# Kernel tuning notes

Hardware: AMD Instinct MI355X
Metric: run time of the kernel (lower is better)

Reference implementation:

```python
import jax, jax.numpy as jnp
import numpy as np

B, D = 8, 128
CH = [1, 2, 4, 8, 16, 32, 64]
STRIDES = [1, 2, 2, 2, 2, 2]
EPS = 1e-5


def setup_inputs() -> dict:
    key = jax.random.key(0)
    ks = jax.random.split(key, 8)
    inp = {
        'x_feats': jax.random.normal(ks[0], (B, D, D, D, 1), jnp.float32),
        'x_mask': jax.random.randint(ks[1], (B, D, D, D, 1), 0, 2).astype(jnp.int32),
    }
    for i in range(6):
        cin, cout = CH[i], CH[i + 1]
        inp[f'w{i}'] = jax.random.normal(ks[2 + i], (3, 3, 3, cin, cout), jnp.float32) * (1.0 / np.sqrt(27.0 * cin))
        inp[f'g{i}'] = jnp.ones((cout,), jnp.float32)
        inp[f'b{i}'] = jnp.zeros((cout,), jnp.float32)
    return inp


def _conv(x, w, stride):
    # x: [B,D,D,D,Cin], w: [3,3,3,Cin,Cout]; SAME-style pad=1 so output index p gathers stride*p + {-1,0,1}
    return jax.lax.conv_general_dilated(
        x, w, (stride,) * 3, [(1, 1)] * 3,
        dimension_numbers=('NDHWC', 'DHWIO', 'NDHWC'))


def _down_mask(m):
    # ME strided coord map: out coord p active iff any input coord c with floor(c/2)==p is active
    return jax.lax.reduce_window(m, 0.0, jax.lax.max,
                                 (1, 2, 2, 2, 1), (1, 2, 2, 2, 1), 'VALID')


def _bn_relu(x, m, g, b):
    # batch-norm over ACTIVE voxels only (x is already zero at inactive sites)
    cnt = jnp.maximum(jnp.sum(m), 1.0)
    mean = jnp.sum(x, axis=(0, 1, 2, 3)) / cnt            # [C]
    var = jnp.sum(x * x, axis=(0, 1, 2, 3)) / cnt - mean * mean
    y = (x - mean) * (g * jax.lax.rsqrt(var + EPS)) + b
    return jnp.maximum(y, 0.0) * m


def _forward(x_feats, x_mask, ws, gs, bs):
    m = x_mask.astype(x_feats.dtype)
    x = x_feats * m
    for i in range(6):
        x = _conv(x, ws[i], STRIDES[i])
        if STRIDES[i] == 2:
            m = _down_mask(m)
        x = x * m  # zero values at inactive output coords (sparse tensor semantics)
        x = _bn_relu(x, m, gs[i], bs[i])
    # sparse max pooling k=3 s=2: max over active inputs in footprint 2p+{-1,0,1}
    neg = jnp.asarray(-jnp.inf, x.dtype)
    filled = jnp.where(m > 0, x, neg)
    pooled = jax.lax.reduce_window(filled, neg, jax.lax.max,
                                   (1, 3, 3, 3, 1), (1, 2, 2, 2, 1),
                                   [(0, 0), (1, 1), (1, 1), (1, 1), (0, 0)])
    mo = _down_mask(m)
    return jnp.where(mo > 0, pooled, 0.0)  # [B, 2, 2, 2, 64]


def reference(x_feats, x_mask, w0, w1, w2, w3, w4, w5,
              g0, g1, g2, g3, g4, g5, b0, b1, b2, b3, b4, b5):
    ws = [w0, w1, w2, w3, w4, w5]
    gs = [g0, g1, g2, g3, g4, g5]
    bs = [b0, b1, b2, b3, b4, b5]
    return _forward(x_feats, x_mask, ws, gs, bs)
```

## Files before the change

### kernel.cpp

```cpp
#include <hip/hip_runtime.h>
#include <hip/hip_bf16.h>
#include <stdint.h>

#define DEV __device__ __forceinline__

constexpr int BATCH = 8;

constexpr int il2(int n) { return (n <= 1) ? 0 : 1 + il2(n / 2); }

DEV float ldy(const float* p, int i) { return p[i]; }
DEV float ldy(const __hip_bfloat16* p, int i) { return __bfloat162float(p[i]); }
DEV void sty(float* p, size_t i, float v) { p[i] = v; }
DEV void sty(__hip_bfloat16* p, size_t i, float v) { p[i] = __float2bfloat16(v); }

DEV uint32_t f2bf(float v) {
  __hip_bfloat16 h = __float2bfloat16(v);
  return (uint32_t)*reinterpret_cast<uint16_t*>(&h);
}
DEV float bflo(uint32_t u) {
  uint32_t t = u << 16;
  float f;
  __builtin_memcpy(&f, &t, 4);
  return f;
}
DEV float bfhi(uint32_t u) {
  uint32_t t = u & 0xffff0000u;
  float f;
  __builtin_memcpy(&f, &t, 4);
  return f;
}
constexpr uint32_t NEGINF_BF = 0xFF80u;
DEV int xswz(int o, int nwg) { return (o & 7) * (nwg >> 3) + (o >> 3); }

__global__ __launch_bounds__(256) void maskA_k(const int* __restrict__ msk,
                                               uint8_t* __restrict__ m0,
                                               uint8_t* __restrict__ m1,
                                               uint8_t* __restrict__ m2) {
  __shared__ uint8_t t0[32768];
  __shared__ uint8_t t1[4096];
  int blk = blockIdx.x;
  int bx = (blk & 3) * 32, by = ((blk >> 2) & 3) * 32, bz = ((blk >> 4) & 3) * 32, b = blk >> 6;
  int tid = threadIdx.x;
  for (int g = tid; g < 8192; g += 256) {
    int gx4 = (g & 7) * 4, gy = (g >> 3) & 31, gz = g >> 8;
    int gidx = ((b * 128 + bz + gz) * 128 + by + gy) * 128 + bx + gx4;
    int4 v = *(const int4*)(msk + gidx);
    uint32_t o = (v.x ? 1u : 0u) | (v.y ? 256u : 0u) | (v.z ? 65536u : 0u) | (v.w ? 16777216u : 0u);
    ((uint32_t*)t0)[g] = o;
    ((uint32_t*)m0)[gidx >> 2] = o;
  }
  __syncthreads();
  for (int j = tid; j < 4096; j += 256) {
    int ox = j & 15, oy = (j >> 4) & 15, oz = j >> 8;
    uint32_t act = 0;
#pragma unroll
    for (int dz = 0; dz < 2; dz++)
#pragma unroll
      for (int dy = 0; dy < 2; dy++)
        act |= *(const uint16_t*)&t0[(2 * oz + dz) * 1024 + (2 * oy + dy) * 32 + 2 * ox];
    uint8_t vv = act ? 1 : 0;
    t1[j] = vv;
    m1[((b * 64 + bz / 2 + oz) * 64 + by / 2 + oy) * 64 + bx / 2 + ox] = vv;
  }
  __syncthreads();
  for (int j = tid; j < 512; j += 256) {
    int ox = j & 7, oy = (j >> 3) & 7, oz = j >> 6;
    uint32_t act = 0;
#pragma unroll
    for (int dz = 0; dz < 2; dz++)
#pragma unroll
      for (int dy = 0; dy < 2; dy++)
        act |= *(const uint16_t*)&t1[(2 * oz + dz) * 256 + (2 * oy + dy) * 16 + 2 * ox];
    m2[((b * 32 + bz / 4 + oz) * 32 + by / 4 + oy) * 32 + bx / 4 + ox] = act ? 1 : 0;
  }
}

__global__ __launch_bounds__(1024) void maskB_k(const uint8_t* __restrict__ m2,
                                                uint8_t* __restrict__ m3,
                                                uint8_t* __restrict__ m4,
                                                uint8_t* __restrict__ m5,
                                                uint8_t* __restrict__ m6) {
  __shared__ uint8_t t3[32768];
  __shared__ uint8_t t4[4096];
  __shared__ uint8_t t5[512];
  int tid = threadIdx.x;
  for (int j = tid; j < 32768; j += 1024) {
    int ox = j & 15, oy = (j >> 4) & 15, oz = (j >> 8) & 15, b = j >> 12;
    uint32_t act = 0;
#pragma unroll
    for (int dz = 0; dz < 2; dz++)
#pragma unroll
      for (int dy = 0; dy < 2; dy++)
        act |= *(const uint16_t*)&m2[((b * 32 + 2 * oz + dz) * 32 + 2 * oy + dy) * 32 + 2 * ox];
    uint8_t v = act ? 1 : 0;
    t3[j] = v;
    m3[j] = v;
  }
  __syncthreads();
  for (int j = tid; j < 4096; j += 1024) {
    int ox = j & 7, oy = (j >> 3) & 7, oz = (j >> 6) & 7, b = j >> 9;
    uint32_t act = 0;
#pragma unroll
    for (int dz = 0; dz < 2; dz++)
#pragma unroll
      for (int dy = 0; dy < 2; dy++)
        act |= *(const uint16_t*)&t3[((b * 16 + 2 * oz + dz) * 16 + 2 * oy + dy) * 16 + 2 * ox];
    uint8_t v = act ? 1 : 0;
    t4[j] = v;
    m4[j] = v;
  }
  __syncthreads();
  if (tid < 512) {
    int j = tid;
    int ox = j & 3, oy = (j >> 2) & 3, oz = (j >> 4) & 3, b = j >> 6;
    uint32_t act = 0;
#pragma unroll
    for (int dz = 0; dz < 2; dz++)
#pragma unroll
      for (int dy = 0; dy < 2; dy++)
        act |= *(const uint16_t*)&t4[((b * 8 + 2 * oz + dz) * 8 + 2 * oy + dy) * 8 + 2 * ox];
    uint8_t v = act ? 1 : 0;
    t5[j] = v;
    m5[j] = v;
  }
  __syncthreads();
  if (tid < 64) {
    int j = tid;
    int ox = j & 1, oy = (j >> 1) & 1, oz = (j >> 2) & 1, b = j >> 3;
    uint32_t act = 0;
#pragma unroll
    for (int dz = 0; dz < 2; dz++)
#pragma unroll
      for (int dy = 0; dy < 2; dy++)
        act |= *(const uint16_t*)&t5[((b * 4 + 2 * oz + dz) * 4 + 2 * oy + dy) * 4 + 2 * ox];
    m6[j] = act ? 1 : 0;
  }
}

__global__ __launch_bounds__(256, 4) void conv0_k(const float* __restrict__ x,
                                                  const uint8_t* __restrict__ m0,
                                                  const float* __restrict__ w,
                                                  __hip_bfloat16* __restrict__ y0,
                                                  float* __restrict__ partials) {
  constexpr int NROW = 180;
  constexpr int ROUNDS = 6;
  __shared__ float sx[3240];
  __shared__ float sm[4][5];
  int blk = xswz(blockIdx.x, 8192);
  int tx0 = (blk & 7) * 16, ty0 = ((blk >> 3) & 7) * 16, tz0 = ((blk >> 6) & 15) * 8,
      b = blk >> 10;
  int tid = threadIdx.x;
  int q = tid & 7, rowb = tid >> 3;

  float4 xq[ROUNDS];
  uint32_t mq[ROUNDS];
#pragma unroll
  for (int r = 0; r < ROUNDS; r++) {
    int row = rowb + 32 * r;
    int sz = row / 18;
    int sy = row - sz * 18;
    int gz = tz0 + sz - 1, gy = ty0 + sy - 1;
    int gx4 = tx0 - 4 + 4 * q;
    bool in = (row < NROW) & ((unsigned)gz < 128u) & ((unsigned)gy < 128u) &
              ((unsigned)gx4 < 128u);
    int gi = in ? ((b * 128 + gz) * 128 + gy) * 128 + gx4 : 0;
    xq[r] = *(const float4*)(x + gi);
    uint32_t mr = *(const uint32_t*)(m0 + gi);
    mq[r] = in ? mr : 0u;
  }
#pragma unroll
  for (int r = 0; r < ROUNDS; r++) {
    int row = rowb + 32 * r;
    if (row >= NROW) continue;
    float vals[4] = {xq[r].x, xq[r].y, xq[r].z, xq[r].w};
    uint32_t mw = mq[r];
#pragma unroll
    for (int e = 0; e < 4; e++) {
      int col = 4 * q - 3 + e;
      if ((unsigned)col < 18u)
        sx[row * 18 + col] = ((mw >> (8 * e)) & 0xffu) ? vals[e] : 0.f;
    }
  }
  __syncthreads();

  int tc = tid & 7, tb = (tid >> 3) & 7, ta = tid >> 6;
  int lx = tc * 2, ly = tb * 2, lz = ta * 2;

  uint32_t mm[2][2];
#pragma unroll
  for (int oz = 0; oz < 2; oz++)
#pragma unroll
    for (int oy = 0; oy < 2; oy++) {
      int z = tz0 + lz + oz, y = ty0 + ly + oy, xx = tx0 + lx;
      mm[oz][oy] = *(const uint16_t*)(m0 + ((b * 128 + z) * 128 + y) * 128 + xx);
    }

  float acc[2][2][2][2];
#pragma unroll
  for (int oz = 0; oz < 2; oz++)
#pragma unroll
    for (int oy = 0; oy < 2; oy++)
#pragma unroll
      for (int ox = 0; ox < 2; ox++)
        acc[oz][oy][ox][0] = acc[oz][oy][ox][1] = 0.f;

#pragma unroll
  for (int p = 0; p < 4; p++) {
    float pl[4][4];
#pragma unroll
    for (int yy = 0; yy < 4; yy++)
#pragma unroll
      for (int xx2 = 0; xx2 < 4; xx2 += 2) {
        float2 v = *(const float2*)&sx[(lz + p) * 324 + (ly + yy) * 18 + lx + xx2];
        pl[yy][xx2] = v.x;
        pl[yy][xx2 + 1] = v.y;
      }
#pragma unroll
    for (int oz = 0; oz < 2; oz++) {
      int dz = p - oz;
      if (dz < 0 || dz > 2) continue;
#pragma unroll
      for (int dy = 0; dy < 3; dy++)
#pragma unroll
        for (int dx = 0; dx < 3; dx++) {
          float w0 = w[((dz * 3 + dy) * 3 + dx) * 2];
          float w1 = w[((dz * 3 + dy) * 3 + dx) * 2 + 1];
#pragma unroll
          for (int oy = 0; oy < 2; oy++)
#pragma unroll
            for (int ox = 0; ox < 2; ox++) {
              float s = pl[oy + dy][ox + dx];
              acc[oz][oy][ox][0] = fmaf(s, w0, acc[oz][oy][ox][0]);
              acc[oz][oy][ox][1] = fmaf(s, w1, acc[oz][oy][ox][1]);
            }
        }
    }
  }

  float s0 = 0.f, q0 = 0.f, s1 = 0.f, q1 = 0.f;
  int cnt = 0;
#pragma unroll
  for (int oz = 0; oz < 2; oz++)
#pragma unroll
    for (int oy = 0; oy < 2; oy++) {
      int z = tz0 + lz + oz, y = ty0 + ly + oy, xx = tx0 + lx;
      int vo = ((b * 128 + z) * 128 + y) * 128 + xx;
      uint32_t m2b = mm[oz][oy];
      uint2 st;
      if (m2b & 0xff) {
        st.x = f2bf(acc[oz][oy][0][0]) | (f2bf(acc[oz][oy][0][1]) << 16);
        s0 += acc[oz][oy][0][0];
        q0 += acc[oz][oy][0][0] * acc[oz][oy][0][0];
        s1 += acc[oz][oy][0][1];
        q1 += acc[oz][oy][0][1] * acc[oz][oy][0][1];
        cnt++;
      } else {
        st.x = NEGINF_BF | (NEGINF_BF << 16);
      }
      if (m2b >> 8) {
        st.y = f2bf(acc[oz][oy][1][0]) | (f2bf(acc[oz][oy][1][1]) << 16);
        s0 += acc[oz][oy][1][0];
        q0 += acc[oz][oy][1][0] * acc[oz][oy][1][0];
        s1 += acc[oz][oy][1][1];
        q1 += acc[oz][oy][1][1] * acc[oz][oy][1][1];
        cnt++;
      } else {
        st.y = NEGINF_BF | (NEGINF_BF << 16);
      }
      ((uint2*)y0)[vo >> 1] = st;
    }
  float cf = (float)cnt;
#pragma unroll
  for (int off = 32; off >= 1; off >>= 1) {
    s0 += __shfl_xor(s0, off);
    q0 += __shfl_xor(q0, off);
    s1 += __shfl_xor(s1, off);
    q1 += __shfl_xor(q1, off);
    cf += __shfl_xor(cf, off);
  }
  int wave = tid >> 6;
  if ((tid & 63) == 0) {
    sm[wave][0] = s0;
    sm[wave][1] = q0;
    sm[wave][2] = s1;
    sm[wave][3] = q1;
    sm[wave][4] = cf;
  }
  __syncthreads();
  if (tid < 5) {
    float t = 0.f;
#pragma unroll
    for (int wv = 0; wv < 4; wv++) t += sm[wv][tid];
    partials[blk * 5 + tid] = t;
  }
}

template <int Din, int Cin, int Cout, int TZ, typename Tin, typename Tout>
__global__ __launch_bounds__(64 * TZ, 4) void conv_tile_k(const Tin* __restrict__ yin,
                                                          const uint8_t* __restrict__ mo,
                                                          const float* __restrict__ ssin,
                                                          const float* __restrict__ w,
                                                          Tout* __restrict__ yout,
                                                          float* __restrict__ partials) {
  static_assert(sizeof(Tin) == 2 && (Cin == 2 || Cin == 4), "bf16 input only");
  constexpr int Dout = Din / 2;
  constexpr int NT = 64 * TZ;
  constexpr int IZ = 2 * TZ + 1;
  constexpr int NROW = 17 * IZ;
  constexpr int NPAIR = NROW * 9;
  constexpr int PR = (NPAIR + NT - 1) / NT;
  constexpr int TXN = Dout / 8;
  constexpr int TZN = Dout / TZ;
  constexpr int LTX = il2(TXN);
  constexpr int LTZ = il2(TZN);
  constexpr int NWG = TXN * TXN * TZN * BATCH;
  constexpr int REC = 2 * Cout + 1;
  __shared__ float sx[289 * IZ * Cin];
  __shared__ float sm[TZ][REC];

  int tid = threadIdx.x;
  int blk = xswz(blockIdx.x, NWG);
  int tx0 = (blk & (TXN - 1)) * 8;
  int ty0 = ((blk >> LTX) & (TXN - 1)) * 8;
  int tz0 = ((blk >> (2 * LTX)) & (TZN - 1)) * TZ;
  int b = blk >> (2 * LTX + LTZ);

  float sc[Cin], sh[Cin];
#pragma unroll
  for (int ci = 0; ci < Cin; ci++) {
    sc[ci] = ssin[2 * ci];
    sh[ci] = ssin[2 * ci + 1];
  }

  int oy0 = 2 * ty0 - 1, oz0 = 2 * tz0 - 1;
  uint2 pv2[PR];
  uint4 pv4[PR];
  uint32_t okb = 0;
#pragma unroll
  for (int r = 0; r < PR; r++) {
    int i = tid + r * NT;
    int row = i / 9, qq = i - 9 * row;
    int sz = row / 17, sy = row - 17 * sz;
    int gz = oz0 + sz, gy = oy0 + sy;
    int px = 2 * tx0 - 2 + 2 * qq;
    bool ok = (i < NPAIR) & ((unsigned)gz < (unsigned)Din) & ((unsigned)gy < (unsigned)Din) &
              (px >= 0);
    int gi = ok ? ((b * Din + gz) * Din + gy) * Din + px : 0;
    if (ok) okb |= (1u << r);
    if constexpr (Cin == 2)
      pv2[r] = *(const uint2*)((const uint16_t*)yin + (size_t)gi * 2);
    else
      pv4[r] = *(const uint4*)((const uint16_t*)yin + (size_t)gi * 4);
  }
#pragma unroll
  for (int r = 0; r < PR; r++) {
    int i = tid + r * NT;
    if (i >= NPAIR) continue;
    int row = i / 9, qq = i - 9 * row;
    bool ok = (okb >> r) & 1u;
#pragma unroll
    for (int e = 0; e < 2; e++) {
      int u = 2 * qq - 1 + e;
      if ((unsigned)u >= 17u) continue;
      int site = row * 17 + u;
      if constexpr (Cin == 2) {
        uint32_t vv = e ? pv2[r].y : pv2[r].x;
        float f0 = ok ? fmaxf(fmaf(bflo(vv), sc[0], sh[0]), 0.f) : 0.f;
        float f1 = ok ? fmaxf(fmaf(bfhi(vv), sc[1], sh[1]), 0.f) : 0.f;
        *(float2*)&sx[site * 2] = make_float2(f0, f1);
      } else {
        uint32_t va = e ? pv4[r].z : pv4[r].x;
        uint32_t vb = e ? pv4[r].w : pv4[r].y;
        float f0 = ok ? fmaxf(fmaf(bflo(va), sc[0], sh[0]), 0.f) : 0.f;
        float f1 = ok ? fmaxf(fmaf(bfhi(va), sc[1], sh[1]), 0.f) : 0.f;
        float f2 = ok ? fmaxf(fmaf(bflo(vb), sc[2], sh[2]), 0.f) : 0.f;
        float f3 = ok ? fmaxf(fmaf(bfhi(vb), sc[3], sh[3]), 0.f) : 0.f;
        *(float4*)&sx[site * 4] = make_float4(f0, f1, f2, f3);
      }
    }
  }
  __syncthreads();

  int tc = tid & 7, tb = (tid >> 3) & 7, ta = tid >> 6;
  int lx = tc, ly = tb, lz = ta;
  int vo = ((b * Dout + tz0 + lz) * Dout + ty0 + ly) * Dout + tx0 + lx;
  bool act = mo[vo] != 0;
  float acc[Cout];
#pragma unroll
  for (int co = 0; co < Cout; co++) acc[co] = 0.f;
  if (act) {
    int base = ((2 * lz) * 289 + (2 * ly) * 17 + (2 * lx)) * Cin;
#pragma unroll
    for (int dz = 0; dz < 3; dz++)
#pragma unroll
      for (int dy = 0; dy < 3; dy++)
#pragma unroll
        for (int dx = 0; dx < 3; dx++) {
          int off = base + (dz * 289 + dy * 17 + dx) * Cin;
          const float* wp = w + ((dz * 3 + dy) * 3 + dx) * Cin * Cout;
#pragma unroll
          for (int ci = 0; ci < Cin; ci++) {
            float s = sx[off + ci];
#pragma unroll
            for (int co = 0; co < Cout; co++)
              acc[co] = fmaf(s, wp[ci * Cout + co], acc[co]);
          }
        }
  }
  {
    uint32_t pk[Cout / 2];
    if (act) {
#pragma unroll
      for (int k = 0; k < Cout / 2; k++) pk[k] = f2bf(acc[2 * k]) | (f2bf(acc[2 * k + 1]) << 16);
    } else {
#pragma unroll
      for (int k = 0; k < Cout / 2; k++) pk[k] = NEGINF_BF | (NEGINF_BF << 16);
    }
    if constexpr (Cout == 4)
      *(uint2*)((uint16_t*)yout + (size_t)vo * 4) = *(uint2*)pk;
    else if constexpr (Cout == 8)
      *(uint4*)((uint16_t*)yout + (size_t)vo * 8) = *(uint4*)pk;
    else {
#pragma unroll
      for (int k = 0; k < Cout / 2; k++)
        *((uint32_t*)yout + (size_t)vo * (Cout / 2) + k) = pk[k];
    }
  }
  unsigned long long bal = __ballot(act);
  int wave = tid >> 6, lane = tid & 63;
#pragma unroll
  for (int co = 0; co < Cout; co++) {
    float s = acc[co], q = acc[co] * acc[co];
#pragma unroll
    for (int off = 32; off >= 1; off >>= 1) {
      s += __shfl_xor(s, off);
      q += __shfl_xor(q, off);
    }
    if (lane == 0) {
      sm[wave][2 * co] = s;
      sm[wave][2 * co + 1] = q;
    }
  }
  if (lane == 0) sm[wave][2 * Cout] = (float)__popcll(bal);
  __syncthreads();
  if (tid < REC) {
    float t = 0.f;
#pragma unroll
    for (int wv = 0; wv < TZ; wv++) t += sm[wv][tid];
    partials[(size_t)blk * REC + tid] = t;
  }
}

template <int Din, int Cin, int Cout, typename Tin, typename Tout>
__global__ __launch_bounds__(256) void conv_s2_k(const Tin* __restrict__ yin,
                                                 const uint8_t* __restrict__ mo,
                                                 const float* __restrict__ ssin,
                                                 const float* __restrict__ w,
                                                 Tout* __restrict__ yout,
                                                 float* __restrict__ partials) {
  constexpr int Dout = Din / 2;
  constexpr int LD = il2(Dout);
  constexpr int LC = il2(Cout);
  constexpr int REC = 2 * Cout + 1;
  int tid = threadIdx.x;
  int lin = blockIdx.x * 256 + tid;
  int co = lin & (Cout - 1);
  int v = lin >> LC;
  int x = v & (Dout - 1);
  int y = (v >> LD) & (Dout - 1);
  int z = (v >> (2 * LD)) & (Dout - 1);
  int b = v >> (3 * LD);
  bool act = mo[v] != 0;
  float acc = 0.f;
  if (act) {
    for (int dz = 0; dz < 3; dz++) {
      int iz = 2 * z + dz - 1;
      if ((unsigned)iz >= (unsigned)Din) continue;
      for (int dy = 0; dy < 3; dy++) {
        int iy = 2 * y + dy - 1;
        if ((unsigned)iy >= (unsigned)Din) continue;
        for (int dx = 0; dx < 3; dx++) {
          int ix = 2 * x + dx - 1;
          if ((unsigned)ix >= (unsigned)Din) continue;
          int gi = ((b * Din + iz) * Din + iy) * Din + ix;
          const float* wp = w + ((dz * 3 + dy) * 3 + dx) * Cin * Cout + co;
          float f[Cin];
          if constexpr (sizeof(Tin) == 2 && Cin == 8) {
            uint4 rr = *(const uint4*)((const uint16_t*)yin + (size_t)gi * 8);
            f[0] = bflo(rr.x);
            f[1] = bfhi(rr.x);
            f[2] = bflo(rr.y);
            f[3] = bfhi(rr.y);
            f[4] = bflo(rr.z);
            f[5] = bfhi(rr.z);
            f[6] = bflo(rr.w);
            f[7] = bfhi(rr.w);
          } else if constexpr (sizeof(Tin) == 4 && (Cin % 4) == 0) {
            const float* yp = (const float*)yin + (size_t)gi * Cin;
#pragma unroll
            for (int c4 = 0; c4 < Cin; c4 += 4) {
              float4 vv = *(const float4*)(yp + c4);
              f[c4] = vv.x;
              f[c4 + 1] = vv.y;
              f[c4 + 2] = vv.z;
              f[c4 + 3] = vv.w;
            }
          } else {
            const Tin* yp = yin + (size_t)gi * Cin;
#pragma unroll
            for (int ci = 0; ci < Cin; ci++) f[ci] = ldy(yp, ci);
          }
#pragma unroll
          for (int ci = 0; ci < Cin; ci++) {
            float val = fmaxf(fmaf(f[ci], ssin[2 * ci], ssin[2 * ci + 1]), 0.f);
            acc = fmaf(val, wp[ci * Cout], acc);
          }
        }
      }
    }
  }
  sty(yout, (size_t)lin, act ? acc : -INFINITY);
  float s = acc, q = acc * acc;
#pragma unroll
  for (int off = 32; off >= Cout; off >>= 1) {
    s += __shfl_xor(s, off);
    q += __shfl_xor(q, off);
  }
  unsigned long long bal = __ballot(act && co == 0);
  __shared__ float sm[4][REC];
  int wave = tid >> 6, lane = tid & 63;
  if (lane < Cout) {
    sm[wave][2 * lane] = s;
    sm[wave][2 * lane + 1] = q;
  }
  if (lane == 0) sm[wave][2 * Cout] = (float)__popcll(bal);
  __syncthreads();
  if (tid < REC)
    partials[(size_t)blockIdx.x * REC + tid] = sm[0][tid] + sm[1][tid] + sm[2][tid] + sm[3][tid];
}

template <int Cout>
__global__ __launch_bounds__(256) void stats_k(const float* __restrict__ partials, int nblocks,
                                               const float* __restrict__ g,
                                               const float* __restrict__ bb,
                                               float* __restrict__ ss) {
  constexpr int REC = 2 * Cout + 1;
  int c = blockIdx.x, tid = threadIdx.x;
  float s = 0.f, q = 0.f, n = 0.f;
  for (int i = tid; i < nblocks; i += 256) {
    const float* p = partials + (size_t)i * REC;
    s += p[2 * c];
    q += p[2 * c + 1];
    n += p[2 * Cout];
  }
  __shared__ float S[256], Q[256], N[256];
  S[tid] = s;
  Q[tid] = q;
  N[tid] = n;
  __syncthreads();
  for (int st = 128; st > 0; st >>= 1) {
    if (tid < st) {
      S[tid] += S[tid + st];
      Q[tid] += Q[tid + st];
      N[tid] += N[tid + st];
    }
    __syncthreads();
  }
  if (tid == 0) {
    float cnt = fmaxf(N[0], 1.f);
    float mean = S[0] / cnt;
    float var = Q[0] / cnt - mean * mean;
    float scale = g[c] * rsqrtf(var + 1e-5f);
    ss[2 * c] = scale;
    ss[2 * c + 1] = bb[c] - mean * scale;
  }
}

__global__ __launch_bounds__(512) void pool_stats_k(const float* __restrict__ y5,
                                                    const uint8_t* __restrict__ m6,
                                                    const float* __restrict__ partials,
                                                    const float* __restrict__ g,
                                                    const float* __restrict__ bb,
                                                    float* __restrict__ out) {
  __shared__ float ssc[64], ssh[64];
  int b = blockIdx.x, tid = threadIdx.x;
  if (tid < 64) {
    float s = 0.f, q = 0.f, n = 0.f;
    for (int i = 0; i < 128; i++) {
      const float* p = partials + i * 129;
      s += p[2 * tid];
      q += p[2 * tid + 1];
      n += p[128];
    }
    float cnt = fmaxf(n, 1.f);
    float mean = s / cnt;
    float var = q / cnt - mean * mean;
    float scale = g[tid] * rsqrtf(var + 1e-5f);
    ssc[tid] = scale;
    ssh[tid] = bb[tid] - mean * scale;
  }
  __syncthreads();
  int c = tid & 63, s = tid >> 6;
  int qx = s & 1, qy = (s >> 1) & 1, qz = (s >> 2) & 1;
  int ov = ((b * 2 + qz) * 2 + qy) * 2 + qx;
  float scale = ssc[c], shift = ssh[c];
  float mx = 0.f;
  for (int dz = 0; dz < 3; dz++) {
    int iz = 2 * qz + dz - 1;
    if ((unsigned)iz >= 4u) continue;
    for (int dy = 0; dy < 3; dy++) {
      int iy = 2 * qy + dy - 1;
      if ((unsigned)iy >= 4u) continue;
      for (int dx = 0; dx < 3; dx++) {
        int ix = 2 * qx + dx - 1;
        if ((unsigned)ix >= 4u) continue;
        int gi = ((b * 4 + iz) * 4 + iy) * 4 + ix;
        float val = fmaxf(fmaf(y5[gi * 64 + c], scale, shift), 0.f);
        mx = fmaxf(mx, val);
      }
    }
  }
  out[ov * 64 + c] = m6[ov] ? mx : 0.f;
}

extern "C" void kernel_launch(void* const* d_in, const int* in_sizes, int n_in,
                              void* d_out, int out_size, void* d_ws, size_t ws_size,
                              hipStream_t stream) {
  const float* x = (const float*)d_in[0];
  const int* msk = (const int*)d_in[1];
  const float *w[6], *g[6], *bb[6];
  for (int i = 0; i < 6; i++) {
    w[i] = (const float*)d_in[2 + 3 * i];
    g[i] = (const float*)d_in[3 + 3 * i];
    bb[i] = (const float*)d_in[4 + 3 * i];
  }

  char* ws = (char*)d_ws;
  size_t o = 0;
  auto A = [&](size_t bytes) -> char* {
    char* p = ws + o;
    o = (o + bytes + 255) & ~(size_t)255;
    return p;
  };
  __hip_bfloat16* y0 = (__hip_bfloat16*)A(33554432 * 2);
  __hip_bfloat16* y1 = (__hip_bfloat16*)A(8388608 * 2);
  __hip_bfloat16* y2 = (__hip_bfloat16*)A(2097152 * 2);
  float* y3 = (float*)A(2097152);
  float* y4 = (float*)A(524288);
  float* y5 = (float*)A(131072);
  uint8_t* m0 = (uint8_t*)A(16777216);
  uint8_t* m1 = (uint8_t*)A(2097152);
  uint8_t* m2 = (uint8_t*)A(262144);
  uint8_t* m3 = (uint8_t*)A(32768);
  uint8_t* m4 = (uint8_t*)A(4096);
  uint8_t* m5 = (uint8_t*)A(512);
  uint8_t* m6 = (uint8_t*)A(64);
  float* part = (float*)A(2 << 20);
  float* ss = (float*)A(4096);
  if (o > ws_size) return;

  maskA_k<<<512, 256, 0, stream>>>(msk, m0, m1, m2);
  maskB_k<<<1, 1024, 0, stream>>>(m2, m3, m4, m5, m6);

  conv0_k<<<8192, 256, 0, stream>>>(x, m0, w[0], y0, part);
  stats_k<2><<<2, 256, 0, stream>>>(part, 8192, g[0], bb[0], ss + 0);
  conv_tile_k<128, 2, 4, 4, __hip_bfloat16, __hip_bfloat16>
      <<<8192, 256, 0, stream>>>(y0, m1, ss + 0, w[1], y1, part);
  stats_k<4><<<4, 256, 0, stream>>>(part, 8192, g[1], bb[1], ss + 128);
  conv_tile_k<64, 4, 8, 4, __hip_bfloat16, __hip_bfloat16>
      <<<1024, 256, 0, stream>>>(y1, m2, ss + 128, w[2], y2, part);
  stats_k<8><<<8, 256, 0, stream>>>(part, 1024, g[2], bb[2], ss + 256);
  conv_s2_k<32, 8, 16, __hip_bfloat16, float>
      <<<2048, 256, 0, stream>>>(y2, m3, ss + 256, w[3], y3, part);
  stats_k<16><<<16, 256, 0, stream>>>(part, 2048, g[3], bb[3], ss + 384);
  conv_s2_k<16, 16, 32, float, float>
      <<<512, 256, 0, stream>>>(y3, m4, ss + 384, w[4], y4, part);
  stats_k<32><<<32, 256, 0, stream>>>(part, 512, g[4], bb[4], ss + 512);
  conv_s2_k<8, 32, 64, float, float>
      <<<128, 256, 0, stream>>>(y4, m5, ss + 512, w[5], y5, part);
  pool_stats_k<<<8, 512, 0, stream>>>(y5, m6, part, g[5], bb[5], (float*)d_out);
}
```

Measured before the change: 254.3 us.

## Fuse BN stats and mask downsampling into producer kernels via last-block atomics

Removes the separate maskB and several stats kernels by having the last-finishing block of each producer kernel, found with fenced atomic counters, compute the coarser masks or the BN scale/shift. This cuts kernel launches and the serial gaps between them in a chain of small kernels. It also rewrites conv0's shared-memory staging with a padded row stride and a different thread-to-load mapping. It adds a memset, atomics and a serial tail in one block per kernel.

```diff
diff --git a/kernel.cpp b/kernel.cpp
--- a/kernel.cpp
+++ b/kernel.cpp
@@ -32,12 +32,57 @@
 constexpr uint32_t NEGINF_BF = 0xFF80u;
 DEV int xswz(int o, int nwg) { return (o & 7) * (nwg >> 3) + (o >> 3); }
 
+template <int Cout>
+DEV void fused_stats_body(const float* partials, int nblocks, const float* g,
+                          const float* bb, float* ss, float* red, int tid) {
+  constexpr int LC = il2(Cout);
+  constexpr int REC = 2 * Cout + 1;
+  int c = tid & (Cout - 1);
+  float s = 0.f, q = 0.f, n = 0.f;
+  for (int i = tid >> LC; i < nblocks; i += (256 >> LC)) {
+    const float* p = partials + (size_t)i * REC;
+    s += p[2 * c];
+    q += p[2 * c + 1];
+    n += p[2 * Cout];
+  }
+  float* S = red;
+  float* Q = red + 256;
+  float* N = red + 512;
+  S[tid] = s;
+  Q[tid] = q;
+  N[tid] = n;
+  __syncthreads();
+  for (int st = 128; st >= Cout; st >>= 1) {
+    if (tid < st) {
+      S[tid] += S[tid + st];
+      Q[tid] += Q[tid + st];
+      N[tid] += N[tid + st];
+    }
+    __syncthreads();
+  }
+  if (tid < Cout) {
+    float cnt = fmaxf(N[tid], 1.f);
+    float mean = S[tid] / cnt;
+    float var = Q[tid] / cnt - mean * mean;
+    float scale = g[tid] * rsqrtf(var + 1e-5f);
+    ss[2 * tid] = scale;
+    ss[2 * tid + 1] = bb[tid] - mean * scale;
+  }
+}
+
 __global__ __launch_bounds__(256) void maskA_k(const int* __restrict__ msk,
                                                uint8_t* __restrict__ m0,
                                                uint8_t* __restrict__ m1,
-                                               uint8_t* __restrict__ m2) {
+                                               uint8_t* __restrict__ m2,
+                                               uint8_t* __restrict__ m3,
+                                               uint8_t* __restrict__ m4,
+                                               uint8_t* __restrict__ m5,
+                                               uint8_t* __restrict__ m6,
+                                               int* __restrict__ cnt) {
   __shared__ uint8_t t0[32768];
   __shared__ uint8_t t1[4096];
+  __shared__ uint8_t t5[512];
+  __shared__ int lastf;
   int blk = blockIdx.x;
   int bx = (blk & 3) * 32, by = ((blk >> 2) & 3) * 32, bz = ((blk >> 4) & 3) * 32, b = blk >> 6;
   int tid = threadIdx.x;
@@ -73,67 +118,68 @@
         act |= *(const uint16_t*)&t1[(2 * oz + dz) * 256 + (2 * oy + dy) * 16 + 2 * ox];
     m2[((b * 32 + bz / 4 + oz) * 32 + by / 4 + oy) * 32 + bx / 4 + ox] = act ? 1 : 0;
   }
-}
-
-__global__ __launch_bounds__(1024) void maskB_k(const uint8_t* __restrict__ m2,
-                                                uint8_t* __restrict__ m3,
-                                                uint8_t* __restrict__ m4,
-                                                uint8_t* __restrict__ m5,
-                                                uint8_t* __restrict__ m6) {
-  __shared__ uint8_t t3[32768];
-  __shared__ uint8_t t4[4096];
-  __shared__ uint8_t t5[512];
-  int tid = threadIdx.x;
-  for (int j = tid; j < 32768; j += 1024) {
-    int ox = j & 15, oy = (j >> 4) & 15, oz = (j >> 8) & 15, b = j >> 12;
-    uint32_t act = 0;
-#pragma unroll
-    for (int dz = 0; dz < 2; dz++)
-#pragma unroll
-      for (int dy = 0; dy < 2; dy++)
-        act |= *(const uint16_t*)&m2[((b * 32 + 2 * oz + dz) * 32 + 2 * oy + dy) * 32 + 2 * ox];
-    uint8_t v = act ? 1 : 0;
-    t3[j] = v;
-    m3[j] = v;
-  }
-  __syncthreads();
-  for (int j = tid; j < 4096; j += 1024) {
-    int ox = j & 7, oy = (j >> 3) & 7, oz = (j >> 6) & 7, b = j >> 9;
-    uint32_t act = 0;
-#pragma unroll
-    for (int dz = 0; dz < 2; dz++)
-#pragma unroll
-      for (int dy = 0; dy < 2; dy++)
-        act |= *(const uint16_t*)&t3[((b * 16 + 2 * oz + dz) * 16 + 2 * oy + dy) * 16 + 2 * ox];
-    uint8_t v = act ? 1 : 0;
-    t4[j] = v;
-    m4[j] = v;
-  }
-  __syncthreads();
-  if (tid < 512) {
-    int j = tid;
-    int ox = j & 3, oy = (j >> 2) & 3, oz = (j >> 4) & 3, b = j >> 6;
-    uint32_t act = 0;
-#pragma unroll
-    for (int dz = 0; dz < 2; dz++)
-#pragma unroll
-      for (int dy = 0; dy < 2; dy++)
-        act |= *(const uint16_t*)&t4[((b * 8 + 2 * oz + dz) * 8 + 2 * oy + dy) * 8 + 2 * ox];
-    uint8_t v = act ? 1 : 0;
-    t5[j] = v;
-    m5[j] = v;
-  }
-  __syncthreads();
-  if (tid < 64) {
-    int j = tid;
-    int ox = j & 1, oy = (j >> 1) & 1, oz = (j >> 2) & 1, b = j >> 3;
-    uint32_t act = 0;
-#pragma unroll
-    for (int dz = 0; dz < 2; dz++)
-#pragma unroll
-      for (int dy = 0; dy < 2; dy++)
-        act |= *(const uint16_t*)&t5[((b * 4 + 2 * oz + dz) * 4 + 2 * oy + dy) * 4 + 2 * ox];
-    m6[j] = act ? 1 : 0;
+  __threadfence();
+  __syncthreads();
+  if (tid == 0) {
+    int d = 0;
+    if (atomicAdd(cnt + 32 * (blk & 7), 1) == (512 >> 3) - 1)
+      d = (atomicAdd(cnt + 256, 1) == 7) ? 1 : 0;
+    lastf = d;
+  }
+  __syncthreads();
+  if (lastf) {
+    __threadfence();
+    for (int j = tid; j < 32768; j += 256) {
+      int ox = j & 15, oy = (j >> 4) & 15, oz = (j >> 8) & 15, bb2 = j >> 12;
+      uint32_t act = 0;
+#pragma unroll
+      for (int dz = 0; dz < 2; dz++)
+#pragma unroll
+        for (int dy = 0; dy < 2; dy++)
+          act |= *(const uint16_t*)&m2[((bb2 * 32 + 2 * oz + dz) * 32 + 2 * oy + dy) * 32 + 2 * ox];
+      uint8_t v = act ? 1 : 0;
+      t0[j] = v;
+      m3[j] = v;
+    }
+    __syncthreads();
+    for (int j = tid; j < 4096; j += 256) {
+      int ox = j & 7, oy = (j >> 3) & 7, oz = (j >> 6) & 7, bb2 = j >> 9;
+      uint32_t act = 0;
+#pragma unroll
+      for (int dz = 0; dz < 2; dz++)
+#pragma unroll
+        for (int dy = 0; dy < 2; dy++)
+          act |= *(const uint16_t*)&t0[((bb2 * 16 + 2 * oz + dz) * 16 + 2 * oy + dy) * 16 + 2 * ox];
+      uint8_t v = act ? 1 : 0;
+      t1[j] = v;
+      m4[j] = v;
+    }
+    __syncthreads();
+    for (int j = tid; j < 512; j += 256) {
+      int ox = j & 3, oy = (j >> 2) & 3, oz = (j >> 4) & 3, bb2 = j >> 6;
+      uint32_t act = 0;
+#pragma unroll
+      for (int dz = 0; dz < 2; dz++)
+#pragma unroll
+        for (int dy = 0; dy < 2; dy++)
+          act |= *(const uint16_t*)&t1[((bb2 * 8 + 2 * oz + dz) * 8 + 2 * oy + dy) * 8 + 2 * ox];
+      uint8_t v = act ? 1 : 0;
+      t5[j] = v;
+      m5[j] = v;
+    }
+    __syncthreads();
+    if (tid < 64) {
+      int j = tid;
+      int ox = j & 1, oy = (j >> 1) & 1, oz = (j >> 2) & 1, bb2 = j >> 3;
+      uint32_t act = 0;
+#pragma unroll
+      for (int dz = 0; dz < 2; dz++)
+#pragma unroll
+        for (int dy = 0; dy < 2; dy++)
+          act |= *(const uint16_t*)&t5[((bb2 * 4 + 2 * oz + dz) * 4 + 2 * oy + dy) * 4 + 2 * ox];
+      m6[j] = act ? 1 : 0;
+    }
+    if (tid < 9) cnt[32 * tid] = 0;
   }
 }
 
@@ -142,43 +188,47 @@
                                                   const float* __restrict__ w,
                                                   __hip_bfloat16* __restrict__ y0,
                                                   float* __restrict__ partials) {
+  constexpr int SR = 26;
   constexpr int NROW = 180;
-  constexpr int ROUNDS = 6;
-  __shared__ float sx[3240];
+  constexpr int NTASK = NROW * 6;
+  constexpr int ROUNDS = 5;
+  __shared__ float sx[NROW * SR];
   __shared__ float sm[4][5];
   int blk = xswz(blockIdx.x, 8192);
   int tx0 = (blk & 7) * 16, ty0 = ((blk >> 3) & 7) * 16, tz0 = ((blk >> 6) & 15) * 8,
       b = blk >> 10;
   int tid = threadIdx.x;
-  int q = tid & 7, rowb = tid >> 3;
 
   float4 xq[ROUNDS];
   uint32_t mq[ROUNDS];
 #pragma unroll
   for (int r = 0; r < ROUNDS; r++) {
-    int row = rowb + 32 * r;
-    int sz = row / 18;
-    int sy = row - sz * 18;
-    int gz = tz0 + sz - 1, gy = ty0 + sy - 1;
-    int gx4 = tx0 - 4 + 4 * q;
-    bool in = (row < NROW) & ((unsigned)gz < 128u) & ((unsigned)gy < 128u) &
+    unsigned i = tid + 256u * r;
+    unsigned row = (i * 43691u) >> 18;
+    int k = (int)(i - row * 6u);
+    unsigned sz = (row * 3641u) >> 16;
+    int sy = (int)(row - sz * 18u);
+    int gz = tz0 + (int)sz - 1, gy = ty0 + sy - 1;
+    int gx4 = tx0 - 4 + 4 * k;
+    bool ok = (row < (unsigned)NROW) & ((unsigned)gz < 128u) & ((unsigned)gy < 128u) &
               ((unsigned)gx4 < 128u);
-    int gi = in ? ((b * 128 + gz) * 128 + gy) * 128 + gx4 : 0;
+    int gi = ok ? ((b * 128 + gz) * 128 + gy) * 128 + gx4 : 0;
     xq[r] = *(const float4*)(x + gi);
     uint32_t mr = *(const uint32_t*)(m0 + gi);
-    mq[r] = in ? mr : 0u;
+    mq[r] = ok ? mr : 0u;
   }
 #pragma unroll
   for (int r = 0; r < ROUNDS; r++) {
-    int row = rowb + 32 * r;
-    if (row >= NROW) continue;
-    float vals[4] = {xq[r].x, xq[r].y, xq[r].z, xq[r].w};
-    uint32_t mw = mq[r];
-#pragma unroll
-    for (int e = 0; e < 4; e++) {
-      int col = 4 * q - 3 + e;
-      if ((unsigned)col < 18u)
-        sx[row * 18 + col] = ((mw >> (8 * e)) & 0xffu) ? vals[e] : 0.f;
+    unsigned i = tid + 256u * r;
+    unsigned row = (i * 43691u) >> 18;
+    int k = (int)(i - row * 6u);
+    if (row < (unsigned)NROW) {
+      float vals[4] = {xq[r].x, xq[r].y, xq[r].z, xq[r].w};
+      uint32_t mw = mq[r];
+      int base = (int)row * SR + 4 * k + 1;
+#pragma unroll
+      for (int e = 0; e < 4; e++)
+        sx[base + e] = ((mw >> (8 * e)) & 0xffu) ? vals[e] : 0.f;
     }
   }
   __syncthreads();
@@ -210,10 +260,10 @@
 #pragma unroll
     for (int yy = 0; yy < 4; yy++)
 #pragma unroll
-      for (int xx2 = 0; xx2 < 4; xx2 += 2) {
-        float2 v = *(const float2*)&sx[(lz + p) * 324 + (ly + yy) * 18 + lx + xx2];
-        pl[yy][xx2] = v.x;
-        pl[yy][xx2 + 1] = v.y;
+      for (int j = 0; j < 4; j += 2) {
+        float2 v = *(const float2*)&sx[((lz + p) * 18 + (ly + yy)) * SR + lx + 4 + j];
+        pl[yy][j] = v.x;
+        pl[yy][j + 1] = v.y;
       }
 #pragma unroll
     for (int oz = 0; oz < 2; oz++) {
@@ -238,7 +288,7 @@
   }
 
   float s0 = 0.f, q0 = 0.f, s1 = 0.f, q1 = 0.f;
-  int cnt = 0;
+  int cnt2 = 0;
 #pragma unroll
   for (int oz = 0; oz < 2; oz++)
 #pragma unroll
@@ -253,7 +303,7 @@
         q0 += acc[oz][oy][0][0] * acc[oz][oy][0][0];
         s1 += acc[oz][oy][0][1];
         q1 += acc[oz][oy][0][1] * acc[oz][oy][0][1];
-        cnt++;
+        cnt2++;
       } else {
         st.x = NEGINF_BF | (NEGINF_BF << 16);
       }
@@ -263,13 +313,13 @@
         q0 += acc[oz][oy][1][0] * acc[oz][oy][1][0];
         s1 += acc[oz][oy][1][1];
         q1 += acc[oz][oy][1][1] * acc[oz][oy][1][1];
-        cnt++;
+        cnt2++;
       } else {
         st.y = NEGINF_BF | (NEGINF_BF << 16);
       }
       ((uint2*)y0)[vo >> 1] = st;
     }
-  float cf = (float)cnt;
+  float cf = (float)cnt2;
 #pragma unroll
   for (int off = 32; off >= 1; off >>= 1) {
     s0 += __shfl_xor(s0, off);
@@ -295,13 +345,17 @@
   }
 }
 
-template <int Din, int Cin, int Cout, int TZ, typename Tin, typename Tout>
+template <int Din, int Cin, int Cout, int TZ, bool FUSE, typename Tin, typename Tout>
 __global__ __launch_bounds__(64 * TZ, 4) void conv_tile_k(const Tin* __restrict__ yin,
                                                           const uint8_t* __restrict__ mo,
                                                           const float* __restrict__ ssin,
                                                           const float* __restrict__ w,
                                                           Tout* __restrict__ yout,
-                                                          float* __restrict__ partials) {
+                                                          float* __restrict__ partials,
+                                                          const float* __restrict__ g,
+                                                          const float* __restrict__ bbv,
+                                                          float* __restrict__ ssout,
+                                                          int* __restrict__ cnt) {
   static_assert(sizeof(Tin) == 2 && (Cin == 2 || Cin == 4), "bf16 input only");
   constexpr int Dout = Din / 2;
   constexpr int NT = 64 * TZ;
@@ -317,6 +371,7 @@
   constexpr int REC = 2 * Cout + 1;
   __shared__ float sx[289 * IZ * Cin];
   __shared__ float sm[TZ][REC];
+  __shared__ int lastf;
 
   int tid = threadIdx.x;
   int blk = xswz(blockIdx.x, NWG);
@@ -449,6 +504,23 @@
     for (int wv = 0; wv < TZ; wv++) t += sm[wv][tid];
     partials[(size_t)blk * REC + tid] = t;
   }
+  if constexpr (FUSE) {
+    __threadfence();
+    __syncthreads();
+    if (tid == 0) {
+      int d = 0;
+      if (atomicAdd(cnt + 32 * (blockIdx.x & 7), 1) == (NWG >> 3) - 1)
+        d = (atomicAdd(cnt + 256, 1) == 7) ? 1 : 0;
+      lastf = d;
+    }
+    __syncthreads();
+    if (lastf) {
+      __threadfence();
+      fused_stats_body<Cout>(partials, NWG, g, bbv, ssout, sx, tid);
+      __syncthreads();
+      if (tid < 9) cnt[32 * tid] = 0;
+    }
+  }
 }
 
 template <int Din, int Cin, int Cout, typename Tin, typename Tout>
@@ -457,11 +529,19 @@
                                                  const float* __restrict__ ssin,
                                                  const float* __restrict__ w,
                                                  Tout* __restrict__ yout,
-                                                 float* __restrict__ partials) {
+                                                 float* __restrict__ partials,
+                                                 const float* __restrict__ g,
+                                                 const float* __restrict__ bbv,
+                                                 float* __restrict__ ssout,
+                                                 int* __restrict__ cnt) {
   constexpr int Dout = Din / 2;
   constexpr int LD = il2(Dout);
   constexpr int LC = il2(Cout);
   constexpr int REC = 2 * Cout + 1;
+  constexpr int NWG = Dout * Dout * Dout * BATCH * Cout / 256;
+  __shared__ float red[768];
+  __shared__ float sm[4][REC];
+  __shared__ int lastf;
   int tid = threadIdx.x;
   int lin = blockIdx.x * 256 + tid;
   int co = lin & (Cout - 1);
@@ -527,7 +607,6 @@
     q += __shfl_xor(q, off);
   }
   unsigned long long bal = __ballot(act && co == 0);
-  __shared__ float sm[4][REC];
   int wave = tid >> 6, lane = tid & 63;
   if (lane < Cout) {
     sm[wave][2 * lane] = s;
@@ -537,6 +616,21 @@
   __syncthreads();
   if (tid < REC)
     partials[(size_t)blockIdx.x * REC + tid] = sm[0][tid] + sm[1][tid] + sm[2][tid] + sm[3][tid];
+  __threadfence();
+  __syncthreads();
+  if (tid == 0) {
+    int d = 0;
+    if (atomicAdd(cnt + 32 * (blockIdx.x & 7), 1) == (NWG >> 3) - 1)
+      d = (atomicAdd(cnt + 256, 1) == 7) ? 1 : 0;
+    lastf = d;
+  }
+  __syncthreads();
+  if (lastf) {
+    __threadfence();
+    fused_stats_body<Cout>(partials, NWG, g, bbv, ssout, red, tid);
+    __syncthreads();
+    if (tid < 9) cnt[32 * tid] = 0;
+  }
 }
 
 template <int Cout>
@@ -576,34 +670,15 @@
   }
 }
 
-__global__ __launch_bounds__(512) void pool_stats_k(const float* __restrict__ y5,
-                                                    const uint8_t* __restrict__ m6,
-                                                    const float* __restrict__ partials,
-                                                    const float* __restrict__ g,
-                                                    const float* __restrict__ bb,
-                                                    float* __restrict__ out) {
-  __shared__ float ssc[64], ssh[64];
+__global__ __launch_bounds__(512) void pool_k(const float* __restrict__ y5,
+                                              const uint8_t* __restrict__ m6,
+                                              const float* __restrict__ ss,
+                                              float* __restrict__ out) {
   int b = blockIdx.x, tid = threadIdx.x;
-  if (tid < 64) {
-    float s = 0.f, q = 0.f, n = 0.f;
-    for (int i = 0; i < 128; i++) {
-      const float* p = partials + i * 129;
-      s += p[2 * tid];
-      q += p[2 * tid + 1];
-      n += p[128];
-    }
-    float cnt = fmaxf(n, 1.f);
-    float mean = s / cnt;
-    float var = q / cnt - mean * mean;
-    float scale = g[tid] * rsqrtf(var + 1e-5f);
-    ssc[tid] = scale;
-    ssh[tid] = bb[tid] - mean * scale;
-  }
-  __syncthreads();
   int c = tid & 63, s = tid >> 6;
   int qx = s & 1, qy = (s >> 1) & 1, qz = (s >> 2) & 1;
   int ov = ((b * 2 + qz) * 2 + qy) * 2 + qx;
-  float scale = ssc[c], shift = ssh[c];
+  float scale = ss[2 * c], shift = ss[2 * c + 1];
   float mx = 0.f;
   for (int dz = 0; dz < 3; dz++) {
     int iz = 2 * qz + dz - 1;
@@ -657,26 +732,31 @@
   uint8_t* m6 = (uint8_t*)A(64);
   float* part = (float*)A(2 << 20);
   float* ss = (float*)A(4096);
+  int* cntbase = (int*)A(10240);
   if (o > ws_size) return;
-
-  maskA_k<<<512, 256, 0, stream>>>(msk, m0, m1, m2);
-  maskB_k<<<1, 1024, 0, stream>>>(m2, m3, m4, m5, m6);
+  int* cntA = cntbase;
+  int* cntC2 = cntbase + 512;
+  int* cntC3 = cntbase + 1024;
+  int* cntC4 = cntbase + 1536;
+  int* cntC5 = cntbase + 2048;
+
+  hipMemsetAsync(cntbase, 0, 10240, stream);
+
+  maskA_k<<<512, 256, 0, stream>>>(msk, m0, m1, m2, m3, m4, m5, m6, cntA);
 
   conv0_k<<<8192, 256, 0, stream>>>(x, m0, w[0], y0, part);
   stats_k<2><<<2, 256, 0, stream>>>(part, 8192, g[0], bb[0], ss + 0);
-  conv_tile_k<128, 2, 4, 4, __hip_bfloat16, __hip_bfloat16>
-      <<<8192, 256, 0, stream>>>(y0, m1, ss + 0, w[1], y1, part);
+  conv_tile_k<128, 2, 4, 4, false, __hip_bfloat16, __hip_bfloat16>
+      <<<8192, 256, 0, stream>>>(y0, m1, ss + 0, w[1], y1, part, nullptr, nullptr, nullptr,
+                                 nullptr);
   stats_k<4><<<4, 256, 0, stream>>>(part, 8192, g[1], bb[1], ss + 128);
-  conv_tile_k<64, 4, 8, 4, __hip_bfloat16, __hip_bfloat16>
-      <<<1024, 256, 0, stream>>>(y1, m2, ss + 128, w[2], y2, part);
-  stats_k<8><<<8, 256, 0, stream>>>(part, 1024, g[2], bb[2], ss + 256);
+  conv_tile_k<64, 4, 8, 4, true, __hip_bfloat16, __hip_bfloat16>
+      <<<1024, 256, 0, stream>>>(y1, m2, ss + 128, w[2], y2, part, g[2], bb[2], ss + 256, cntC2);
   conv_s2_k<32, 8, 16, __hip_bfloat16, float>
-      <<<2048, 256, 0, stream>>>(y2, m3, ss + 256, w[3], y3, part);
-  stats_k<16><<<16, 256, 0, stream>>>(part, 2048, g[3], bb[3], ss + 384);
+      <<<2048, 256, 0, stream>>>(y2, m3, ss + 256, w[3], y3, part, g[3], bb[3], ss + 384, cntC3);
   conv_s2_k<16, 16, 32, float, float>
-      <<<512, 256, 0, stream>>>(y3, m4, ss + 384, w[4], y4, part);
-  stats_k<32><<<32, 256, 0, stream>>>(part, 512, g[4], bb[4], ss + 512);
+      <<<512, 256, 0, stream>>>(y3, m4, ss + 384, w[4], y4, part, g[4], bb[4], ss + 512, cntC4);
   conv_s2_k<8, 32, 64, float, float>
-      <<<128, 256, 0, stream>>>(y4, m5, ss + 512, w[5], y5, part);
-  pool_stats_k<<<8, 512, 0, stream>>>(y5, m6, part, g[5], bb[5], (float*)d_out);
-}
+      <<<128, 256, 0, stream>>>(y4, m5, ss + 512, w[5], y5, part, g[5], bb[5], ss + 640, cntC5);
+  pool_k<<<8, 512, 0, stream>>>(y5, m6, ss + 640, (float*)d_out);
+}
```

New measurement: 602.2 us. +136.8%, slower.
